# Kernel tuning notes

Measured on AMD Instinct MI355X. Metric: run time of the kernel, lower is better.

The kernel has to match this reference:

```python
import jax, jax.numpy as jnp
import numpy as np

B, C, HW, SCALE = 8, 512, 64, 8
M = C // SCALE  # Q/K channel dim
EPS = 1e-6


def setup_inputs() -> dict:
    key = jax.random.key(0)
    ks = jax.random.split(key, 8)
    s = 0.02
    return {
        "x": jax.random.normal(ks[0], (B, C, HW, HW), dtype=jnp.float32),
        "wq": jax.random.normal(ks[1], (M, C), dtype=jnp.float32) * s,
        "bq": jax.random.normal(ks[2], (M,), dtype=jnp.float32) * s,
        "wk": jax.random.normal(ks[3], (M, C), dtype=jnp.float32) * s,
        "bk": jax.random.normal(ks[4], (M,), dtype=jnp.float32) * s,
        "wv": jax.random.normal(ks[5], (C, C), dtype=jnp.float32) * s,
        "bv": jax.random.normal(ks[6], (C,), dtype=jnp.float32) * s,
        "gamma": jax.random.normal(ks[7], (1,), dtype=jnp.float32),
    }


def reference(x, wq, bq, wk, bk, wv, bv, gamma):
    b, c, w, h = x.shape
    n = w * h
    xf = x.reshape(b, c, n)  # [B,C,N]
    # 1x1 convs == channel GEMMs
    Q = jnp.einsum('bcn,mc->bmn', xf, wq) + bq[None, :, None]  # [B,M,N]
    K = jnp.einsum('bcn,mc->bmn', xf, wk) + bk[None, :, None]  # [B,M,N]
    V = jnp.einsum('bcn,oc->bon', xf, wv) + bv[None, :, None]  # [B,C,N]
    # pooling gate: global max + global avg over spatial dims -> [B,C,1]
    gate = (jnp.max(xf, axis=-1) + jnp.mean(xf, axis=-1))[:, :, None]
    V = gate * V
    Qf = jax.nn.softplus(Q).transpose(0, 2, 1)  # [B,N,M]
    Kf = jax.nn.softplus(K)                      # [B,M,N]
    KV = jnp.einsum('bmn,bcn->bmc', Kf, V)       # [B,M,C]
    norm = 1.0 / jnp.einsum('bnm,bm->bn', Qf, jnp.sum(Kf, axis=-1) + EPS)  # [B,N]
    wval = jnp.einsum('bnm,bmc,bn->bcn', Qf, KV, norm)  # [B,C,N]
    wval = wval.reshape(b, c, h, w)
    return x + gamma * wval
```

## Files before the change

kernel.cpp:

```cpp
#include <hip/hip_runtime.h>
#include <math.h>

#define Bb 8
#define Cc 512
#define Nn 4096
#define Mm 64
#define OC 640
#define EPSf 1e-6f

typedef unsigned short ushort_t;
typedef unsigned int uint_t;
typedef __attribute__((ext_vector_type(8))) short short8;
typedef __attribute__((ext_vector_type(4))) float f32x4;

constexpr size_t OFF_GATE = 0;
constexpr size_t OFF_BCAT = OFF_GATE + (size_t)Bb * Cc;
constexpr size_t OFF_GPM  = OFF_BCAT + (size_t)OC;
constexpr size_t OFF_GPS  = OFF_GPM + (size_t)64 * Bb * Cc;
constexpr size_t OFF_WBF  = OFF_GPS + (size_t)64 * Bb * Cc;
constexpr size_t OFF_XT   = OFF_WBF + (size_t)OC * Cc / 2;
constexpr size_t OFF_QBF  = OFF_XT + (size_t)Bb * Nn * Cc / 2;
constexpr size_t OFF_KBF  = OFF_QBF + (size_t)Bb * Mm * Nn / 2;
constexpr size_t OFF_VBF  = OFF_KBF + (size_t)Bb * Mm * Nn / 2;
constexpr size_t OFF_KVBF = OFF_VBF + (size_t)Bb * Cc * Nn / 2;
constexpr size_t OFF_KSUM = OFF_KVBF + (size_t)Bb * Cc * Mm / 2;
constexpr size_t OFF_NORM = OFF_KSUM + (size_t)Bb * Mm;
constexpr size_t OFF_QT   = OFF_NORM + (size_t)Bb * Nn;

__device__ __forceinline__ float softplus_f(float v) {
    return fmaxf(v, 0.f) + __logf(1.f + __expf(-fabsf(v)));
}
__device__ __forceinline__ ushort_t f2bf(float f) {
    uint_t u = __float_as_uint(f);
    uint_t r = (u + 0x7fffu + ((u >> 16) & 1u)) >> 16;
    return (ushort_t)r;
}
__device__ __forceinline__ float bf2f(ushort_t h) {
    return __uint_as_float(((uint_t)h) << 16);
}
__device__ __forceinline__ void gload_lds16(const void* g, void* l) {
    __builtin_amdgcn_global_load_lds(
        (const __attribute__((address_space(1))) unsigned int*)g,
        (__attribute__((address_space(3))) unsigned int*)l, 16, 0, 0);
}
#define BARRIER()   asm volatile("s_barrier" ::: "memory")
#define WAIT_VM(N)  asm volatile("s_waitcnt vmcnt(" #N ")" ::: "memory")

__global__ void wconv_k(const float* __restrict__ wq, const float* __restrict__ bq,
                        const float* __restrict__ wk, const float* __restrict__ bk,
                        const float* __restrict__ wv, const float* __restrict__ bv,
                        ushort_t* __restrict__ wbf, float* __restrict__ bcat) {
    int i = blockIdx.x * 256 + threadIdx.x;
    if (i < OC * Cc) {
        int o = i / Cc, c = i % Cc;
        float v;
        if (o < Mm)            v = wq[o * Cc + c];
        else if (o < 2 * Mm)   v = wk[(o - Mm) * Cc + c];
        else                   v = wv[(o - 2 * Mm) * Cc + c];
        wbf[i] = f2bf(v);
    }
    if (i < OC) {
        float v;
        if (i < Mm)            v = bq[i];
        else if (i < 2 * Mm)   v = bk[i - Mm];
        else                   v = bv[i - 2 * Mm];
        bcat[i] = v;
    }
}

__global__ __launch_bounds__(256) void xtrans_k(const float* __restrict__ x, ushort_t* __restrict__ xT,
                                                float* __restrict__ gpm, float* __restrict__ gps) {
    const int nb = blockIdx.x * 64;
    const int cb = blockIdx.y * 64;
    const int b  = blockIdx.z;
    __shared__ float Xt[64][65];
    __shared__ float pmx[4][64], psm[4][64];
    const int t = threadIdx.x;
    #pragma unroll
    for (int r = 0; r < 16; r++) {
        int cl = (t >> 6) + r * 4;
        int nl = t & 63;
        Xt[cl][nl] = x[((size_t)b * Cc + cb + cl) * Nn + nb + nl];
    }
    __syncthreads();
    #pragma unroll
    for (int r = 0; r < 8; r++) {
        int nl = (t >> 5) + r * 8;
        int c0 = (t & 31) * 2;
        uint_t pk = (uint_t)f2bf(Xt[c0][nl]) | ((uint_t)f2bf(Xt[c0 + 1][nl]) << 16);
        *(uint_t*)(xT + ((size_t)b * Nn + nb + nl) * Cc + cb + c0) = pk;
    }
    {
        int cl = t & 63, q = t >> 6;
        float mx = -3.4e38f, sm = 0.f;
        #pragma unroll
        for (int j = 0; j < 16; j++) {
            float v = Xt[cl][q * 16 + j];
            mx = fmaxf(mx, v); sm += v;
        }
        pmx[q][cl] = mx; psm[q][cl] = sm;
    }
    __syncthreads();
    if (t < 64) {
        float mx = fmaxf(fmaxf(pmx[0][t], pmx[1][t]), fmaxf(pmx[2][t], pmx[3][t]));
        float sm = psm[0][t] + psm[1][t] + psm[2][t] + psm[3][t];
        size_t idx = (size_t)blockIdx.x * (Bb * Cc) + (size_t)b * Cc + cb + t;
        gpm[idx] = mx;
        gps[idx] = sm;
    }
}

__global__ void gatered_k(const float* __restrict__ gpm, const float* __restrict__ gps,
                          float* __restrict__ gate) {
    int bc = blockIdx.x;
    int l = threadIdx.x;
    float mx = gpm[(size_t)l * (Bb * Cc) + bc];
    float sm = gps[(size_t)l * (Bb * Cc) + bc];
    #pragma unroll
    for (int off = 32; off; off >>= 1) {
        mx = fmaxf(mx, __shfl_xor(mx, off));
        sm += __shfl_xor(sm, off);
    }
    if (l == 0) gate[bc] = mx + sm * (1.f / Nn);
}

__global__ __launch_bounds__(256, 3) void qkv_mfma_k(const ushort_t* __restrict__ wbf,
                                                     const ushort_t* __restrict__ xT,
                                                     const float* __restrict__ bcat,
                                                     const float* __restrict__ gate,
                                                     ushort_t* __restrict__ Qbf,
                                                     ushort_t* __restrict__ Kbf,
                                                     ushort_t* __restrict__ Vbf) {
    const int nb = blockIdx.x * 128;
    const int ob = blockIdx.y * 128;
    const int b  = blockIdx.z;
    __shared__ ushort_t At[2][4096];
    __shared__ ushort_t Bt[2][4096];
    const int tid  = threadIdx.x;
    const int w    = tid >> 6;
    const int lane = tid & 63;
    const int wr   = w >> 1, wc = w & 1;
    const int hi   = lane >> 4, lo = lane & 15;
    const int rwl  = lane >> 2;
    const int kc   = (((lane & 3) ^ ((lane >> 3) & 3)) * 8);
    const int sx   = (hi ^ ((lo >> 1) & 3)) * 8;
    const ushort_t* xb = xT + (size_t)b * Nn * Cc;

    f32x4 acc[4][4] = {};

    auto stage = [&](int buf, int kb) {
        #pragma unroll
        for (int li = 0; li < 2; li++) {
            const int rw = (w * 2 + li) * 16 + rwl;
            gload_lds16(wbf + (size_t)(ob + rw) * Cc + kb + kc, &At[buf][(w * 2 + li) * 512]);
            gload_lds16(xb + (size_t)(nb + rw) * Cc + kb + kc, &Bt[buf][(w * 2 + li) * 512]);
        }
    };
    auto compute = [&](int buf) {
        short8 a[4], bfr[4];
        #pragma unroll
        for (int mi = 0; mi < 4; mi++)
            a[mi] = *(const short8*)(&At[buf][(wr * 64 + mi * 16 + lo) * 32 + sx]);
        #pragma unroll
        for (int ni = 0; ni < 4; ni++)
            bfr[ni] = *(const short8*)(&Bt[buf][(wc * 64 + ni * 16 + lo) * 32 + sx]);
        #pragma unroll
        for (int mi = 0; mi < 4; mi++)
            #pragma unroll
            for (int ni = 0; ni < 4; ni++)
                acc[mi][ni] = __builtin_amdgcn_mfma_f32_16x16x32_bf16(a[mi], bfr[ni], acc[mi][ni], 0, 0, 0);
    };

    stage(0, 0);
    #pragma unroll
    for (int t = 0; t < 16; ++t) {
        if (t < 15) {
            stage((t + 1) & 1, (t + 1) * 32);
            WAIT_VM(4);
        } else {
            WAIT_VM(0);
        }
        BARRIER();
        compute(t & 1);
        BARRIER();
    }

    #pragma unroll
    for (int mi = 0; mi < 4; mi++) {
        #pragma unroll
        for (int r = 0; r < 4; r++) {
            const int o = ob + wr * 64 + mi * 16 + hi * 4 + r;
            const float bias = bcat[o];
            if (o < Mm) {
                ushort_t* dst = Qbf + ((size_t)b * Mm + o) * Nn;
                #pragma unroll
                for (int ni = 0; ni < 4; ni++)
                    dst[nb + wc * 64 + ni * 16 + lo] = f2bf(softplus_f(acc[mi][ni][r] + bias));
            } else if (o < 2 * Mm) {
                ushort_t* dst = Kbf + ((size_t)b * Mm + (o - Mm)) * Nn;
                #pragma unroll
                for (int ni = 0; ni < 4; ni++)
                    dst[nb + wc * 64 + ni * 16 + lo] = f2bf(softplus_f(acc[mi][ni][r] + bias));
            } else {
                const int c = o - 2 * Mm;
                const float g = gate[b * Cc + c];
                ushort_t* dst = Vbf + ((size_t)b * Cc + c) * Nn;
                #pragma unroll
                for (int ni = 0; ni < 4; ni++)
                    dst[nb + wc * 64 + ni * 16 + lo] = f2bf(g * (acc[mi][ni][r] + bias));
            }
        }
    }
}

__global__ __launch_bounds__(256) void ksum_k(const ushort_t* __restrict__ Kbf, float* __restrict__ Ksum) {
    int bm = blockIdx.x;
    const ushort_t* row = Kbf + (size_t)bm * Nn;
    int t = threadIdx.x;
    float sm = 0.f;
    for (int i = t * 8; i < Nn; i += 2048) {
        short8 v = *(const short8*)(row + i);
        #pragma unroll
        for (int j = 0; j < 8; j++) sm += bf2f((ushort_t)v[j]);
    }
    #pragma unroll
    for (int off = 32; off; off >>= 1) sm += __shfl_xor(sm, off);
    __shared__ float ssm[4];
    if ((t & 63) == 0) ssm[t >> 6] = sm;
    __syncthreads();
    if (t == 0) Ksum[bm] = ssm[0] + ssm[1] + ssm[2] + ssm[3];
}

__global__ __launch_bounds__(256, 3) void kv_mfma_k(const ushort_t* __restrict__ Kbf,
                                                    const ushort_t* __restrict__ Vbf,
                                                    float* __restrict__ KVpart) {
    const int cb = blockIdx.x * 128;
    const int split = blockIdx.y;
    const int b = blockIdx.z;
    __shared__ ushort_t Vt[2][4096];
    __shared__ ushort_t Kt[2][2048];
    const int tid = threadIdx.x;
    const int w = tid >> 6, lane = tid & 63;
    const int hi = lane >> 4, lo = lane & 15;
    const int rwl = lane >> 2;
    const int kc  = (((lane & 3) ^ ((lane >> 3) & 3)) * 8);
    const int sx  = (hi ^ ((lo >> 1) & 3)) * 8;
    const ushort_t* Vb = Vbf + (size_t)b * Cc * Nn;
    const ushort_t* Kb = Kbf + (size_t)b * Mm * Nn;
    const int nbase = split * 512;

    f32x4 acc[2][4] = {};

    auto stage = [&](int buf, int n0) {
        #pragma unroll
        for (int li = 0; li < 2; li++) {
            const int rw = (w * 2 + li) * 16 + rwl;
            gload_lds16(Vb + (size_t)(cb + rw) * Nn + n0 + kc, &Vt[buf][(w * 2 + li) * 512]);
        }
        gload_lds16(Kb + (size_t)(w * 16 + rwl) * Nn + n0 + kc, &Kt[buf][w * 512]);
    };
    auto compute = [&](int buf) {
        short8 a[2], bv[4];
        #pragma unroll
        for (int mi = 0; mi < 2; mi++)
            a[mi] = *(const short8*)(&Vt[buf][(w * 32 + mi * 16 + lo) * 32 + sx]);
        #pragma unroll
        for (int ni = 0; ni < 4; ni++)
            bv[ni] = *(const short8*)(&Kt[buf][(ni * 16 + lo) * 32 + sx]);
        #pragma unroll
        for (int mi = 0; mi < 2; mi++)
            #pragma unroll
            for (int ni = 0; ni < 4; ni++)
                acc[mi][ni] = __builtin_amdgcn_mfma_f32_16x16x32_bf16(a[mi], bv[ni], acc[mi][ni], 0, 0, 0);
    };

    stage(0, nbase);
    #pragma unroll
    for (int t = 0; t < 16; ++t) {
        if (t < 15) {
            stage((t + 1) & 1, nbase + (t + 1) * 32);
            WAIT_VM(3);
        } else {
            WAIT_VM(0);
        }
        BARRIER();
        compute(t & 1);
        BARRIER();
    }

    float* dst = KVpart + (size_t)(split * Bb + b) * Cc * Mm;
    #pragma unroll
    for (int mi = 0; mi < 2; mi++)
        #pragma unroll
        for (int r = 0; r < 4; r++) {
            const int c = cb + w * 32 + mi * 16 + hi * 4 + r;
            #pragma unroll
            for (int ni = 0; ni < 4; ni++)
                dst[(size_t)c * Mm + ni * 16 + lo] = acc[mi][ni][r];
        }
}

__global__ __launch_bounds__(256) void kvred_k(const float* __restrict__ KVpart, ushort_t* __restrict__ KVbf) {
    int i = blockIdx.x * 256 + threadIdx.x;
    const f32x4* p = (const f32x4*)KVpart;
    f32x4 s = p[i];
    #pragma unroll
    for (int sp = 1; sp < 8; sp++) s += p[(size_t)sp * 65536 + i];
    uint2 pk;
    pk.x = (uint_t)f2bf(s[0]) | ((uint_t)f2bf(s[1]) << 16);
    pk.y = (uint_t)f2bf(s[2]) | ((uint_t)f2bf(s[3]) << 16);
    *(uint2*)(KVbf + (size_t)i * 4) = pk;
}

__global__ __launch_bounds__(256) void qtransnorm_k(const ushort_t* __restrict__ Qbf,
                                                    const float* __restrict__ Ksum,
                                                    ushort_t* __restrict__ QT,
                                                    float* __restrict__ normb) {
    const int n0 = blockIdx.x * 64;
    const int b  = blockIdx.y;
    __shared__ float Qs[64][65];
    __shared__ float ks[64];
    __shared__ float ps[4][64];
    const int t = threadIdx.x;
    if (t < 64) ks[t] = Ksum[b * Mm + t] + EPSf;
    {
        int m = t >> 2, q = t & 3;
        const ushort_t* src = Qbf + ((size_t)b * Mm + m) * Nn + n0 + q * 16;
        short8 v0 = *(const short8*)(src);
        short8 v1 = *(const short8*)(src + 8);
        #pragma unroll
        for (int j = 0; j < 8; j++) {
            Qs[m][q * 16 + j]     = bf2f((ushort_t)v0[j]);
            Qs[m][q * 16 + 8 + j] = bf2f((ushort_t)v1[j]);
        }
    }
    __syncthreads();
    {
        int n = t & 63, ch = t >> 6;
        float s = 0.f;
        #pragma unroll
        for (int j = 0; j < 16; j++) s += Qs[ch * 16 + j][n] * ks[ch * 16 + j];
        ps[ch][n] = s;
    }
    __syncthreads();
    if (t < 64) normb[(size_t)b * Nn + n0 + t] = 1.f / (ps[0][t] + ps[1][t] + ps[2][t] + ps[3][t]);
    #pragma unroll
    for (int i = 0; i < 2; i++) {
        int u = t + i * 256;
        int n = u >> 3, j = u & 7;
        short8 v;
        #pragma unroll
        for (int jj = 0; jj < 8; jj++) v[jj] = (short)f2bf(Qs[j * 8 + jj][n]);
        *(short8*)(QT + ((size_t)b * Nn + n0 + n) * Mm + j * 8) = v;
    }
}

__global__ __launch_bounds__(256, 2) void final_mfma_k(const float* __restrict__ x,
                                                       const ushort_t* __restrict__ QT,
                                                       const ushort_t* __restrict__ KVbf,
                                                       const float* __restrict__ normb,
                                                       const float* __restrict__ gamma,
                                                       float* __restrict__ out) {
    const int nb = blockIdx.x * 128;
    const int cb = blockIdx.y * 128;
    const int b  = blockIdx.z;
    __shared__ ushort_t Qs[128 * 64];
    __shared__ ushort_t Ks[128 * 64];
    const int tid  = threadIdx.x;
    const int w    = tid >> 6;
    const int lane = tid & 63;
    const int wr   = w >> 1, wc = w & 1;
    const int hi   = lane >> 4, lo = lane & 15;
    const int lr   = lane >> 3;
    const int swz  = (((lane & 7) ^ (lr & 7)) * 8);
    const ushort_t* Qb = QT + (size_t)b * Nn * Mm;
    const ushort_t* Kb = KVbf + (size_t)b * Cc * Mm;

    #pragma unroll
    for (int p = 0; p < 4; p++) {
        const int rb = p * 32 + w * 8;
        gload_lds16(Qb + (size_t)(nb + rb + lr) * Mm + swz, &Qs[rb * 64]);
        gload_lds16(Kb + (size_t)(cb + rb + lr) * Mm + swz, &Ks[rb * 64]);
    }
    __syncthreads();

    f32x4 acc[4][4] = {};
    #pragma unroll
    for (int kk = 0; kk < 2; kk++) {
        short8 a[4], bfr[4];
        #pragma unroll
        for (int mi = 0; mi < 4; mi++) {
            const int row = wr * 64 + mi * 16 + lo;
            a[mi] = *(const short8*)(&Qs[row * 64 + (((kk * 4 + hi) ^ (lo & 7)) * 8)]);
        }
        #pragma unroll
        for (int ni = 0; ni < 4; ni++) {
            const int row = wc * 64 + ni * 16 + lo;
            bfr[ni] = *(const short8*)(&Ks[row * 64 + (((kk * 4 + hi) ^ (lo & 7)) * 8)]);
        }
        #pragma unroll
        for (int mi = 0; mi < 4; mi++)
            #pragma unroll
            for (int ni = 0; ni < 4; ni++)
                acc[mi][ni] = __builtin_amdgcn_mfma_f32_16x16x32_bf16(a[mi], bfr[ni], acc[mi][ni], 0, 0, 0);
    }

    const float g = gamma[0];
    #pragma unroll
    for (int mi = 0; mi < 4; mi++) {
        const int n0 = nb + wr * 64 + mi * 16 + hi * 4;
        float4 nrm = *(const float4*)(normb + (size_t)b * Nn + n0);
        #pragma unroll
        for (int ni = 0; ni < 4; ni++) {
            const int c = cb + wc * 64 + ni * 16 + lo;
            size_t idx = ((size_t)b * Cc + c) * Nn + n0;
            float4 xv = *(const float4*)(x + idx);
            float4 o;
            o.x = xv.x + g * nrm.x * acc[mi][ni][0];
            o.y = xv.y + g * nrm.y * acc[mi][ni][1];
            o.z = xv.z + g * nrm.z * acc[mi][ni][2];
            o.w = xv.w + g * nrm.w * acc[mi][ni][3];
            *(float4*)(out + idx) = o;
        }
    }
}

extern "C" void kernel_launch(void* const* d_in, const int* in_sizes, int n_in,
                              void* d_out, int out_size, void* d_ws, size_t ws_size,
                              hipStream_t stream) {
    const float* x     = (const float*)d_in[0];
    const float* wq    = (const float*)d_in[1];
    const float* bq    = (const float*)d_in[2];
    const float* wk    = (const float*)d_in[3];
    const float* bk    = (const float*)d_in[4];
    const float* wv    = (const float*)d_in[5];
    const float* bv    = (const float*)d_in[6];
    const float* gamma = (const float*)d_in[7];
    float* out = (float*)d_out;
    float* ws  = (float*)d_ws;

    float*    gate   = ws + OFF_GATE;
    float*    bcat   = ws + OFF_BCAT;
    float*    gpm    = ws + OFF_GPM;
    float*    gps    = ws + OFF_GPS;
    ushort_t* wbf    = (ushort_t*)(ws + OFF_WBF);
    ushort_t* xT     = (ushort_t*)(ws + OFF_XT);
    float*    KVpart = ws + OFF_XT;
    ushort_t* Qbf    = (ushort_t*)(ws + OFF_QBF);
    ushort_t* Kbf    = (ushort_t*)(ws + OFF_KBF);
    ushort_t* Vbf    = (ushort_t*)(ws + OFF_VBF);
    ushort_t* KVbf   = (ushort_t*)(ws + OFF_KVBF);
    float*    Ksum   = ws + OFF_KSUM;
    float*    normb  = ws + OFF_NORM;
    ushort_t* QT     = (ushort_t*)(ws + OFF_QT);

    wconv_k<<<(OC * Cc + 255) / 256, 256, 0, stream>>>(wq, bq, wk, bk, wv, bv, wbf, bcat);
    xtrans_k<<<dim3(Nn / 64, Cc / 64, Bb), 256, 0, stream>>>(x, xT, gpm, gps);
    gatered_k<<<Bb * Cc, 64, 0, stream>>>(gpm, gps, gate);
    qkv_mfma_k<<<dim3(Nn / 128, OC / 128, Bb), 256, 0, stream>>>(wbf, xT, bcat, gate, Qbf, Kbf, Vbf);
    ksum_k<<<Bb * Mm, 256, 0, stream>>>(Kbf, Ksum);
    kv_mfma_k<<<dim3(Cc / 128, 8, Bb), 256, 0, stream>>>(Kbf, Vbf, KVpart);
    kvred_k<<<(Bb * Cc * Mm / 4) / 256, 256, 0, stream>>>(KVpart, KVbf);
    qtransnorm_k<<<dim3(Nn / 64, Bb), 256, 0, stream>>>(Qbf, Ksum, QT, normb);
    final_mfma_k<<<dim3(Nn / 128, Cc / 128, Bb), 256, 0, stream>>>(x, QT, KVbf, normb, gamma, out);
}
```

Before: 114.2 us.

## Use single-wave 64x64 QKV tiles without barriers and fold gate into KV reduce

Result: slower. 124.2 us (+8.7%).

```diff
diff --git a/kernel.cpp b/kernel.cpp
--- a/kernel.cpp
+++ b/kernel.cpp
@@ -124,46 +124,47 @@
     if (l == 0) gate[bc] = mx + sm * (1.f / Nn);
 }
 
-__global__ __launch_bounds__(256, 3) void qkv_mfma_k(const ushort_t* __restrict__ wbf,
-                                                     const ushort_t* __restrict__ xT,
-                                                     const float* __restrict__ bcat,
-                                                     const float* __restrict__ gate,
-                                                     ushort_t* __restrict__ Qbf,
-                                                     ushort_t* __restrict__ Kbf,
-                                                     ushort_t* __restrict__ Vbf) {
-    const int nb = blockIdx.x * 128;
-    const int ob = blockIdx.y * 128;
+__global__ __launch_bounds__(64) void qkv_mfma_k(const ushort_t* __restrict__ wbf,
+                                                 const ushort_t* __restrict__ xT,
+                                                 const float* __restrict__ bcat,
+                                                 ushort_t* __restrict__ Qbf,
+                                                 ushort_t* __restrict__ Kbf,
+                                                 ushort_t* __restrict__ Vbf) {
+    const int nb = blockIdx.x * 64;
+    const int ot = blockIdx.y;
     const int b  = blockIdx.z;
-    __shared__ ushort_t At[2][4096];
-    __shared__ ushort_t Bt[2][4096];
-    const int tid  = threadIdx.x;
-    const int w    = tid >> 6;
-    const int lane = tid & 63;
-    const int wr   = w >> 1, wc = w & 1;
-    const int hi   = lane >> 4, lo = lane & 15;
-    const int rwl  = lane >> 2;
-    const int kc   = (((lane & 3) ^ ((lane >> 3) & 3)) * 8);
-    const int sx   = (hi ^ ((lo >> 1) & 3)) * 8;
+    __shared__ ushort_t At[2][2048];
+    __shared__ ushort_t Bt[2][2048];
+    const int lane = threadIdx.x;
+    const int hi = lane >> 4, lo = lane & 15;
+    const int rwl = lane >> 2;
+    const int kc  = (((lane & 3) ^ ((lane >> 3) & 3)) * 8);
+    const int sx  = (hi ^ ((lo >> 1) & 3)) * 8;
     const ushort_t* xb = xT + (size_t)b * Nn * Cc;
+    const ushort_t* wb = wbf + (size_t)ot * 64 * Cc;
 
     f32x4 acc[4][4] = {};
 
     auto stage = [&](int buf, int kb) {
         #pragma unroll
-        for (int li = 0; li < 2; li++) {
-            const int rw = (w * 2 + li) * 16 + rwl;
-            gload_lds16(wbf + (size_t)(ob + rw) * Cc + kb + kc, &At[buf][(w * 2 + li) * 512]);
-            gload_lds16(xb + (size_t)(nb + rw) * Cc + kb + kc, &Bt[buf][(w * 2 + li) * 512]);
+        for (int li = 0; li < 4; li++) {
+            const int rw = li * 16 + rwl;
+            gload_lds16(wb + (size_t)rw * Cc + kb + kc, &At[buf][li * 512]);
+        }
+        #pragma unroll
+        for (int li = 0; li < 4; li++) {
+            const int rw = li * 16 + rwl;
+            gload_lds16(xb + (size_t)(nb + rw) * Cc + kb + kc, &Bt[buf][li * 512]);
         }
     };
     auto compute = [&](int buf) {
         short8 a[4], bfr[4];
         #pragma unroll
         for (int mi = 0; mi < 4; mi++)
-            a[mi] = *(const short8*)(&At[buf][(wr * 64 + mi * 16 + lo) * 32 + sx]);
+            a[mi] = *(const short8*)(&At[buf][(mi * 16 + lo) * 32 + sx]);
         #pragma unroll
         for (int ni = 0; ni < 4; ni++)
-            bfr[ni] = *(const short8*)(&Bt[buf][(wc * 64 + ni * 16 + lo) * 32 + sx]);
+            bfr[ni] = *(const short8*)(&Bt[buf][(ni * 16 + lo) * 32 + sx]);
         #pragma unroll
         for (int mi = 0; mi < 4; mi++)
             #pragma unroll
@@ -174,42 +175,45 @@
     stage(0, 0);
     #pragma unroll
     for (int t = 0; t < 16; ++t) {
+        __builtin_amdgcn_sched_barrier(0);
         if (t < 15) {
             stage((t + 1) & 1, (t + 1) * 32);
-            WAIT_VM(4);
+            WAIT_VM(8);
         } else {
             WAIT_VM(0);
         }
-        BARRIER();
         compute(t & 1);
-        BARRIER();
-    }
-
-    #pragma unroll
-    for (int mi = 0; mi < 4; mi++) {
-        #pragma unroll
-        for (int r = 0; r < 4; r++) {
-            const int o = ob + wr * 64 + mi * 16 + hi * 4 + r;
-            const float bias = bcat[o];
-            if (o < Mm) {
-                ushort_t* dst = Qbf + ((size_t)b * Mm + o) * Nn;
+    }
+
+    ushort_t* dst0;
+    if (ot == 0)      dst0 = Qbf + (size_t)b * Mm * Nn;
+    else if (ot == 1) dst0 = Kbf + (size_t)b * Mm * Nn;
+    else              dst0 = Vbf + ((size_t)b * Cc + (ot - 2) * 64) * Nn;
+
+    if (ot < 2) {
+        #pragma unroll
+        for (int mi = 0; mi < 4; mi++)
+            #pragma unroll
+            for (int r = 0; r < 4; r++) {
+                const int ol = mi * 16 + hi * 4 + r;
+                const float bias = bcat[ot * 64 + ol];
+                ushort_t* dst = dst0 + (size_t)ol * Nn + nb;
                 #pragma unroll
                 for (int ni = 0; ni < 4; ni++)
-                    dst[nb + wc * 64 + ni * 16 + lo] = f2bf(softplus_f(acc[mi][ni][r] + bias));
-            } else if (o < 2 * Mm) {
-                ushort_t* dst = Kbf + ((size_t)b * Mm + (o - Mm)) * Nn;
+                    dst[ni * 16 + lo] = f2bf(softplus_f(acc[mi][ni][r] + bias));
+            }
+    } else {
+        #pragma unroll
+        for (int mi = 0; mi < 4; mi++)
+            #pragma unroll
+            for (int r = 0; r < 4; r++) {
+                const int ol = mi * 16 + hi * 4 + r;
+                const float bias = bcat[ot * 64 + ol];
+                ushort_t* dst = dst0 + (size_t)ol * Nn + nb;
                 #pragma unroll
                 for (int ni = 0; ni < 4; ni++)
-                    dst[nb + wc * 64 + ni * 16 + lo] = f2bf(softplus_f(acc[mi][ni][r] + bias));
-            } else {
-                const int c = o - 2 * Mm;
-                const float g = gate[b * Cc + c];
-                ushort_t* dst = Vbf + ((size_t)b * Cc + c) * Nn;
-                #pragma unroll
-                for (int ni = 0; ni < 4; ni++)
-                    dst[nb + wc * 64 + ni * 16 + lo] = f2bf(g * (acc[mi][ni][r] + bias));
+                    dst[ni * 16 + lo] = f2bf(acc[mi][ni][r] + bias);
             }
-        }
     }
 }
 
@@ -300,15 +304,21 @@
         }
 }
 
-__global__ __launch_bounds__(256) void kvred_k(const float* __restrict__ KVpart, ushort_t* __restrict__ KVbf) {
+__global__ __launch_bounds__(256) void kvred_k(const float* __restrict__ KVpart,
+                                               const float* __restrict__ gate,
+                                               ushort_t* __restrict__ KVbf) {
     int i = blockIdx.x * 256 + threadIdx.x;
     const f32x4* p = (const f32x4*)KVpart;
     f32x4 s = p[i];
     #pragma unroll
     for (int sp = 1; sp < 8; sp++) s += p[(size_t)sp * 65536 + i];
+    int idx4 = i * 4;
+    int b = idx4 >> 15;
+    int c = (idx4 >> 6) & (Cc - 1);
+    float g = gate[b * Cc + c];
     uint2 pk;
-    pk.x = (uint_t)f2bf(s[0]) | ((uint_t)f2bf(s[1]) << 16);
-    pk.y = (uint_t)f2bf(s[2]) | ((uint_t)f2bf(s[3]) << 16);
+    pk.x = (uint_t)f2bf(s[0] * g) | ((uint_t)f2bf(s[1] * g) << 16);
+    pk.y = (uint_t)f2bf(s[2] * g) | ((uint_t)f2bf(s[3] * g) << 16);
     *(uint2*)(KVbf + (size_t)i * 4) = pk;
 }
 
@@ -457,10 +467,10 @@
     wconv_k<<<(OC * Cc + 255) / 256, 256, 0, stream>>>(wq, bq, wk, bk, wv, bv, wbf, bcat);
     xtrans_k<<<dim3(Nn / 64, Cc / 64, Bb), 256, 0, stream>>>(x, xT, gpm, gps);
     gatered_k<<<Bb * Cc, 64, 0, stream>>>(gpm, gps, gate);
-    qkv_mfma_k<<<dim3(Nn / 128, OC / 128, Bb), 256, 0, stream>>>(wbf, xT, bcat, gate, Qbf, Kbf, Vbf);
+    qkv_mfma_k<<<dim3(Nn / 64, OC / 64, Bb), 64, 0, stream>>>(wbf, xT, bcat, Qbf, Kbf, Vbf);
     ksum_k<<<Bb * Mm, 256, 0, stream>>>(Kbf, Ksum);
     kv_mfma_k<<<dim3(Cc / 128, 8, Bb), 256, 0, stream>>>(Kbf, Vbf, KVpart);
-    kvred_k<<<(Bb * Cc * Mm / 4) / 256, 256, 0, stream>>>(KVpart, KVbf);
+    kvred_k<<<(Bb * Cc * Mm / 4) / 256, 256, 0, stream>>>(KVpart, gate, KVbf);
     qtransnorm_k<<<dim3(Nn / 64, Bb), 256, 0, stream>>>(Qbf, Ksum, QT, normb);
     final_mfma_k<<<dim3(Nn / 128, Cc / 128, Bb), 256, 0, stream>>>(x, QT, KVbf, normb, gamma, out);
 }
```

## Fuse K-sum into QKV GEMM, move gate to KV reduce, triple-buffer loads

Applied to the files above, without the earlier changes.

New measurement: 123.5 us. +8.1%, slower.

```diff
diff --git a/kernel.cpp b/kernel.cpp
--- a/kernel.cpp
+++ b/kernel.cpp
@@ -127,15 +127,15 @@
 __global__ __launch_bounds__(256, 3) void qkv_mfma_k(const ushort_t* __restrict__ wbf,
                                                      const ushort_t* __restrict__ xT,
                                                      const float* __restrict__ bcat,
-                                                     const float* __restrict__ gate,
                                                      ushort_t* __restrict__ Qbf,
                                                      ushort_t* __restrict__ Kbf,
-                                                     ushort_t* __restrict__ Vbf) {
+                                                     ushort_t* __restrict__ Vbf,
+                                                     float* __restrict__ Ksum) {
     const int nb = blockIdx.x * 128;
     const int ob = blockIdx.y * 128;
     const int b  = blockIdx.z;
-    __shared__ ushort_t At[2][4096];
-    __shared__ ushort_t Bt[2][4096];
+    __shared__ ushort_t At[3][4096];
+    __shared__ ushort_t Bt[3][4096];
     const int tid  = threadIdx.x;
     const int w    = tid >> 6;
     const int lane = tid & 63;
@@ -172,17 +172,13 @@
     };
 
     stage(0, 0);
+    stage(1, 32);
     #pragma unroll
     for (int t = 0; t < 16; ++t) {
-        if (t < 15) {
-            stage((t + 1) & 1, (t + 1) * 32);
-            WAIT_VM(4);
-        } else {
-            WAIT_VM(0);
-        }
+        if (t < 15) { WAIT_VM(4); } else { WAIT_VM(0); }
         BARRIER();
-        compute(t & 1);
-        BARRIER();
+        if (t + 2 < 16) stage((t + 2) % 3, (t + 2) * 32);
+        compute(t % 3);
     }
 
     #pragma unroll
@@ -192,43 +188,31 @@
             const int o = ob + wr * 64 + mi * 16 + hi * 4 + r;
             const float bias = bcat[o];
             if (o < Mm) {
-                ushort_t* dst = Qbf + ((size_t)b * Mm + o) * Nn;
+                ushort_t* dst = Qbf + ((size_t)b * Mm + o) * Nn + nb + wc * 64;
                 #pragma unroll
                 for (int ni = 0; ni < 4; ni++)
-                    dst[nb + wc * 64 + ni * 16 + lo] = f2bf(softplus_f(acc[mi][ni][r] + bias));
+                    dst[ni * 16 + lo] = f2bf(softplus_f(acc[mi][ni][r] + bias));
             } else if (o < 2 * Mm) {
-                ushort_t* dst = Kbf + ((size_t)b * Mm + (o - Mm)) * Nn;
+                ushort_t* dst = Kbf + ((size_t)b * Mm + (o - Mm)) * Nn + nb + wc * 64;
+                float s = 0.f;
+                #pragma unroll
+                for (int ni = 0; ni < 4; ni++) {
+                    float sp = softplus_f(acc[mi][ni][r] + bias);
+                    dst[ni * 16 + lo] = f2bf(sp);
+                    s += sp;
+                }
+                s += __shfl_xor(s, 1); s += __shfl_xor(s, 2);
+                s += __shfl_xor(s, 4); s += __shfl_xor(s, 8);
+                if (lo == 0) atomicAdd(&Ksum[b * Mm + (o - Mm)], s);
+            } else {
+                const int c = o - 2 * Mm;
+                ushort_t* dst = Vbf + ((size_t)b * Cc + c) * Nn + nb + wc * 64;
                 #pragma unroll
                 for (int ni = 0; ni < 4; ni++)
-                    dst[nb + wc * 64 + ni * 16 + lo] = f2bf(softplus_f(acc[mi][ni][r] + bias));
-            } else {
-                const int c = o - 2 * Mm;
-                const float g = gate[b * Cc + c];
-                ushort_t* dst = Vbf + ((size_t)b * Cc + c) * Nn;
-                #pragma unroll
-                for (int ni = 0; ni < 4; ni++)
-                    dst[nb + wc * 64 + ni * 16 + lo] = f2bf(g * (acc[mi][ni][r] + bias));
+                    dst[ni * 16 + lo] = f2bf(acc[mi][ni][r] + bias);
             }
         }
     }
-}
-
-__global__ __launch_bounds__(256) void ksum_k(const ushort_t* __restrict__ Kbf, float* __restrict__ Ksum) {
-    int bm = blockIdx.x;
-    const ushort_t* row = Kbf + (size_t)bm * Nn;
-    int t = threadIdx.x;
-    float sm = 0.f;
-    for (int i = t * 8; i < Nn; i += 2048) {
-        short8 v = *(const short8*)(row + i);
-        #pragma unroll
-        for (int j = 0; j < 8; j++) sm += bf2f((ushort_t)v[j]);
-    }
-    #pragma unroll
-    for (int off = 32; off; off >>= 1) sm += __shfl_xor(sm, off);
-    __shared__ float ssm[4];
-    if ((t & 63) == 0) ssm[t >> 6] = sm;
-    __syncthreads();
-    if (t == 0) Ksum[bm] = ssm[0] + ssm[1] + ssm[2] + ssm[3];
 }
 
 __global__ __launch_bounds__(256, 3) void kv_mfma_k(const ushort_t* __restrict__ Kbf,
@@ -300,15 +284,21 @@
         }
 }
 
-__global__ __launch_bounds__(256) void kvred_k(const float* __restrict__ KVpart, ushort_t* __restrict__ KVbf) {
+__global__ __launch_bounds__(256) void kvred_k(const float* __restrict__ KVpart,
+                                               const float* __restrict__ gate,
+                                               ushort_t* __restrict__ KVbf) {
     int i = blockIdx.x * 256 + threadIdx.x;
     const f32x4* p = (const f32x4*)KVpart;
     f32x4 s = p[i];
     #pragma unroll
     for (int sp = 1; sp < 8; sp++) s += p[(size_t)sp * 65536 + i];
+    int idx4 = i * 4;
+    int b = idx4 >> 15;
+    int c = (idx4 >> 6) & (Cc - 1);
+    float g = gate[b * Cc + c];
     uint2 pk;
-    pk.x = (uint_t)f2bf(s[0]) | ((uint_t)f2bf(s[1]) << 16);
-    pk.y = (uint_t)f2bf(s[2]) | ((uint_t)f2bf(s[3]) << 16);
+    pk.x = (uint_t)f2bf(s[0] * g) | ((uint_t)f2bf(s[1] * g) << 16);
+    pk.y = (uint_t)f2bf(s[2] * g) | ((uint_t)f2bf(s[3] * g) << 16);
     *(uint2*)(KVbf + (size_t)i * 4) = pk;
 }
 
@@ -355,7 +345,7 @@
     }
 }
 
-__global__ __launch_bounds__(256, 2) void final_mfma_k(const float* __restrict__ x,
+__global__ __launch_bounds__(256, 4) void final_mfma_k(const float* __restrict__ x,
                                                        const ushort_t* __restrict__ QT,
                                                        const ushort_t* __restrict__ KVbf,
                                                        const float* __restrict__ normb,
@@ -457,10 +447,10 @@
     wconv_k<<<(OC * Cc + 255) / 256, 256, 0, stream>>>(wq, bq, wk, bk, wv, bv, wbf, bcat);
     xtrans_k<<<dim3(Nn / 64, Cc / 64, Bb), 256, 0, stream>>>(x, xT, gpm, gps);
     gatered_k<<<Bb * Cc, 64, 0, stream>>>(gpm, gps, gate);
-    qkv_mfma_k<<<dim3(Nn / 128, OC / 128, Bb), 256, 0, stream>>>(wbf, xT, bcat, gate, Qbf, Kbf, Vbf);
-    ksum_k<<<Bb * Mm, 256, 0, stream>>>(Kbf, Ksum);
+    hipMemsetAsync(Ksum, 0, (size_t)Bb * Mm * sizeof(float), stream);
+    qkv_mfma_k<<<dim3(Nn / 128, OC / 128, Bb), 256, 0, stream>>>(wbf, xT, bcat, Qbf, Kbf, Vbf, Ksum);
     kv_mfma_k<<<dim3(Cc / 128, 8, Bb), 256, 0, stream>>>(Kbf, Vbf, KVpart);
-    kvred_k<<<(Bb * Cc * Mm / 4) / 256, 256, 0, stream>>>(KVpart, KVbf);
+    kvred_k<<<(Bb * Cc * Mm / 4) / 256, 256, 0, stream>>>(KVpart, gate, KVbf);
     qtransnorm_k<<<dim3(Nn / 64, Bb), 256, 0, stream>>>(Qbf, Ksum, QT, normb);
     final_mfma_k<<<dim3(Nn / 128, Cc / 128, Bb), 256, 0, stream>>>(x, QT, KVbf, normb, gamma, out);
 }
```
